# Optimization experiments

Hardware: AMD Instinct MI355X
Metric: run time of the kernel (lower is better)

Reference implementation:

```python
import jax, jax.numpy as jnp
import numpy as np
from jax import lax

D = 256; NH = 8; LYR = 2; G = 64; K = G * G; T = 4; EC = 32
B = 4; N = 512; CITY = 256; DFF = 4 * D

def _conv(x, w):
    return lax.conv_general_dilated(x, w, (1, 1), 'SAME', dimension_numbers=('NCHW', 'OIHW', 'NCHW'))

def _ln(x, w, b):
    m = x.mean(-1, keepdims=True)
    v = ((x - m) ** 2).mean(-1, keepdims=True)
    return (x - m) / jnp.sqrt(v + 1e-5) * w + b

def _mlp(x, w1, b1, w2, b2):
    return jax.nn.gelu(x @ w1 + b1) @ w2 + b2

def setup_inputs():
    key = jax.random.key(0)
    ks = iter(jax.random.split(key, 64))
    def nrm(shape, s=0.02):
        return jax.random.normal(next(ks), shape, jnp.float32) * s
    return {
        'meas_xy': jax.random.uniform(next(ks), (B, N, 2), jnp.float32),
        'meas_v': jax.random.normal(next(ks), (B, N), jnp.float32),
        'bs_xy': jax.random.uniform(next(ks), (B, 1, 2), jnp.float32),
        'task_id': jax.random.randint(next(ks), (B,), 0, T),
        'city': jax.random.uniform(next(ks), (B, CITY, CITY), jnp.float32),
        'mp_w1': nrm((3, D)), 'mp_b1': jnp.zeros((D,)), 'mp_w2': nrm((D, D)), 'mp_b2': jnp.zeros((D,)),
        'bp_w1': nrm((2, D)), 'bp_b1': jnp.zeros((D,)), 'bp_w2': nrm((D, D)), 'bp_b2': jnp.zeros((D,)),
        'env_w1': nrm((EC, 1, 3, 3)), 'env_b1': jnp.zeros((EC,)),
        'env_w2': nrm((EC, EC, 3, 3)), 'env_b2': jnp.zeros((EC,)),
        'env_w3': nrm((D, EC, 1, 1)), 'env_b3': jnp.zeros((D,)),
        'task_emb': nrm((T, D)), 'tp_w': nrm((D, D)), 'tp_b': jnp.zeros((D,)),
        'grid_pos': nrm((K, D)),
        'blk_dens_w': nrm((LYR, D)), 'blk_dens_b': jnp.zeros((LYR, D)),
        'blk_ln1_w': jnp.ones((LYR, D)), 'blk_ln1_b': jnp.zeros((LYR, D)),
        'blk_wq': nrm((LYR, D, D)), 'blk_bq': jnp.zeros((LYR, D)),
        'blk_wk': nrm((LYR, D, D)), 'blk_bk': jnp.zeros((LYR, D)),
        'blk_wv': nrm((LYR, D, D)), 'blk_bv': jnp.zeros((LYR, D)),
        'blk_wo': nrm((LYR, D, D)), 'blk_bo': jnp.zeros((LYR, D)),
        'blk_ln2_w': jnp.ones((LYR, D)), 'blk_ln2_b': jnp.zeros((LYR, D)),
        'blk_ff_w1': nrm((LYR, D, DFF)), 'blk_ff_b1': jnp.zeros((LYR, DFF)),
        'blk_ff_w2': nrm((LYR, DFF, D)), 'blk_ff_b2': jnp.zeros((LYR, D)),
        'tfp_w': nrm((T, D, D)), 'tfp_b': jnp.zeros((T, D)),
        'head_w': nrm((D, 1)), 'head_b': jnp.zeros((1,)),
    }

def reference(meas_xy, meas_v, bs_xy, task_id, city, mp_w1, mp_b1, mp_w2, mp_b2, bp_w1, bp_b1, bp_w2, bp_b2, env_w1, env_b1, env_w2, env_b2, env_w3, env_b3, task_emb, tp_w, tp_b, grid_pos, blk_dens_w, blk_dens_b, blk_ln1_w, blk_ln1_b, blk_wq, blk_bq, blk_wk, blk_bk, blk_wv, blk_bv, blk_wo, blk_bo, blk_ln2_w, blk_ln2_b, blk_ff_w1, blk_ff_b1, blk_ff_w2, blk_ff_b2, tfp_w, tfp_b, head_w, head_b):
    b = meas_xy.shape[0]
    dh = D // NH
    # normalized grid cell centers, [K,2] in (x,y) order
    c = (jnp.arange(G, dtype=jnp.float32) + 0.5) / G
    gy, gx = jnp.meshgrid(c, c, indexing='ij')
    grid_xy = jnp.stack([gx, gy], -1).reshape(K, 2)
    meas_tok = _mlp(jnp.concatenate([meas_xy, meas_v[..., None]], -1), mp_w1, mp_b1, mp_w2, mp_b2)
    bs_tok = _mlp(bs_xy, bp_w1, bp_b1, bp_w2, bp_b2)
    src = jnp.concatenate([meas_tok, bs_tok], 1)       # [B,Ns,D]
    src_xy = jnp.concatenate([meas_xy, bs_xy], 1)      # [B,Ns,2]
    # distance bias: [B,K,Ns]
    attn_bias = -jnp.linalg.norm(grid_xy[None, :, None, :] - src_xy[:, None, :, :], axis=-1)
    # gaussian measurement density: [B,K]
    diff = grid_xy[None, :, None, :] - meas_xy[:, None, :, :]
    dist2 = (diff * diff).sum(-1)
    sigma = 0.08
    density = jnp.exp(-dist2 / (2.0 * sigma * sigma)).mean(-1)
    # env branch: nearest-resize city to GxG, small CNN
    idx = jnp.floor(jnp.arange(G) * (city.shape[1] / G)).astype(jnp.int32)
    city_grid = city[:, idx][:, :, idx][:, None]       # [B,1,G,G]
    h = jax.nn.gelu(_conv(city_grid, env_w1) + env_b1[None, :, None, None])
    h = jax.nn.gelu(_conv(h, env_w2) + env_b2[None, :, None, None])
    env_map = _conv(h, env_w3) + env_b3[None, :, None, None]
    env_grid = env_map.transpose(0, 2, 3, 1).reshape(b, K, D)
    task_vec = (task_emb[task_id] @ tp_w + tp_b)[:, None, :]
    grid = grid_pos[None] + task_vec + env_grid
    inv_sqrt = jnp.float32(1.0 / np.sqrt(dh))
    for l in range(LYR):
        # density modulation injected into the grid latent
        g = grid + density[..., None] * blk_dens_w[l] + blk_dens_b[l]
        hn = _ln(g, blk_ln1_w[l], blk_ln1_b[l])
        q = (hn @ blk_wq[l] + blk_bq[l]).reshape(b, K, NH, dh)
        kk = (src @ blk_wk[l] + blk_bk[l]).reshape(b, -1, NH, dh)
        vv = (src @ blk_wv[l] + blk_bv[l]).reshape(b, -1, NH, dh)
        scores = jnp.einsum('bkhd,bnhd->bhkn', q, kk) * inv_sqrt + attn_bias[:, None]
        a = jax.nn.softmax(scores, -1)
        o = jnp.einsum('bhkn,bnhd->bkhd', a, vv).reshape(b, K, D) @ blk_wo[l] + blk_bo[l]
        g = g + o
        g = g + _mlp(_ln(g, blk_ln2_w[l], blk_ln2_b[l]), blk_ff_w1[l], blk_ff_b1[l], blk_ff_w2[l], blk_ff_b2[l])
        grid = g
    # per-sample task projection from the weight bank
    tf = jax.nn.gelu(jnp.einsum('bkd,bdh->bkh', grid, tfp_w[task_id]) + tfp_b[task_id][:, None, :])
    logits = (tf @ head_w + head_b)[..., 0].reshape(b, G, G)
    return logits
```

## Files before the change

### kernel.cpp

```cpp
#include <hip/hip_runtime.h>
#include <hip/hip_bf16.h>
#include <math.h>

#define D 256
#define NH 8
#define DH 32
#define LYR 2
#define G 64
#define KK 4096
#define T 4
#define EC 32
#define B 4
#define N 512
#define CITY 256
#define DFF 1024
#define NS 513
#define NSP 544
#define MSRC 2052
#define MSRCP 2176
#define ISQ 0.17677669529663687f
#define LOG2E 1.4426950408889634f

typedef short bf16x8 __attribute__((ext_vector_type(8)));
typedef float f32x4 __attribute__((ext_vector_type(4)));

__device__ __forceinline__ float gelu_f(float x) {
    const float c2 = 2.f * 0.7978845608028654f * LOG2E;
    float u = x + 0.044715f * x * x * x;
    float e = __builtin_amdgcn_exp2f(-c2 * u);
    return x * __builtin_amdgcn_rcpf(1.f + e);
}

__device__ __forceinline__ unsigned short f2bf(float f) {
    unsigned int u = __float_as_uint(f);
    unsigned int r = (u + 0x7FFFu + ((u >> 16) & 1u)) >> 16;
    return (unsigned short)r;
}

__device__ __forceinline__ float bf2f(unsigned short u) {
    return __uint_as_float((unsigned)u << 16);
}

__device__ __forceinline__ unsigned cvtpk(float a, float b) {
    unsigned r;
    asm("v_cvt_pk_bf16_f32 %0, %1, %2" : "=v"(r) : "v"(a), "v"(b));
    return r;
}

__device__ __forceinline__ void gl2lds16(const unsigned short* g, unsigned short* l) {
    __builtin_amdgcn_global_load_lds(
        (const __attribute__((address_space(1))) unsigned int*)g,
        (__attribute__((address_space(3))) unsigned int*)l, 16, 0, 0);
}

__global__ __launch_bounds__(256) void pre1_k(
    const float* __restrict__ wq, const float* __restrict__ wk,
    const float* __restrict__ wv, const float* __restrict__ wo,
    const float* __restrict__ ff1, const float* __restrict__ ff2,
    const float* __restrict__ tfp,
    const float* __restrict__ bk, const float* __restrict__ bv,
    unsigned short* __restrict__ wqT, unsigned short* __restrict__ kvT,
    unsigned short* __restrict__ woT, unsigned short* __restrict__ ff1T,
    unsigned short* __restrict__ ff2T, unsigned short* __restrict__ tfpT,
    float* __restrict__ kvbias,
    const float* __restrict__ meas_xy, const float* __restrict__ meas_v,
    const float* __restrict__ bs_xy,
    const float* __restrict__ mp_w1, const float* __restrict__ mp_b1,
    const float* __restrict__ mp_w2, const float* __restrict__ mp_b2,
    const float* __restrict__ bp_w1, const float* __restrict__ bp_b1,
    const float* __restrict__ bp_w2, const float* __restrict__ bp_b2,
    unsigned short* __restrict__ srcbf, float* __restrict__ src_xy,
    float* __restrict__ dens,
    const float* __restrict__ city, const float* __restrict__ env_w1,
    const float* __restrict__ env_b1, float* __restrict__ h1,
    const float* __restrict__ task_emb, const int* __restrict__ task_id,
    const float* __restrict__ tp_w, const float* __restrict__ tp_b,
    float* __restrict__ tvec,
    unsigned short* __restrict__ khd, unsigned short* __restrict__ vch)
{
    __shared__ float sh[1088];
    int bx = blockIdx.x;
    int tid = threadIdx.x;
    if (bx < 1792) {
        const float* src; unsigned short* dst;
        int Kd, Nn, nmat, rowOff = 0, t; size_t matStride;
        if (bx < 512) {
            int job = bx >> 7; t = bx & 127;
            Kd = 256; Nn = 256; nmat = 2;
            if (job == 0)      { src = wq; dst = wqT; matStride = 65536; }
            else if (job == 1) { src = wk; dst = kvT; matStride = 131072; }
            else if (job == 2) { src = wv; dst = kvT; matStride = 131072; rowOff = 256; }
            else               { src = wo; dst = woT; matStride = 65536; }
            if ((t & 63) == 0 && job == 1) kvbias[(t >> 6) * 512 + tid] = bk[(t >> 6) * 256 + tid];
            if ((t & 63) == 0 && job == 2) kvbias[(t >> 6) * 512 + 256 + tid] = bv[(t >> 6) * 256 + tid];
        } else if (bx < 1024) { t = bx - 512;  src = ff1; dst = ff1T; Kd = 256;  Nn = 1024; nmat = 2; matStride = 262144; }
        else if (bx < 1536)   { t = bx - 1024; src = ff2; dst = ff2T; Kd = 1024; Nn = 256;  nmat = 2; matStride = 262144; }
        else                  { t = bx - 1536; src = tfp; dst = tfpT; Kd = 256;  Nn = 256;  nmat = 4; matStride = 65536; }
        int tn = Nn / 32, perMat = tn * (Kd / 32);
        int mat = t / perMat;
        int rem = t - mat * perMat;
        int nb = (rem % tn) * 32, kb = (rem / tn) * 32;
        const float* s = src + (size_t)mat * Kd * Nn;
        unsigned short* d = dst + (size_t)mat * matStride;
        float (*tb)[33] = (float (*)[33])sh;
        int tx = tid & 31, ty = tid >> 5;
        #pragma unroll
        for (int i = 0; i < 4; i++)
            tb[ty + i * 8][tx] = s[(size_t)(kb + ty + i * 8) * Nn + nb + tx];
        __syncthreads();
        #pragma unroll
        for (int i = 0; i < 4; i++)
            d[(size_t)(rowOff + nb + ty + i * 8) * Kd + kb + tx] = f2bf(tb[tx][ty + i * 8]);
    } else if (bx < 3968) {
        int id = bx - 1792;
        int dd = tid;
        if (id >= B * N + B) {
            srcbf[(size_t)id * D + dd] = 0;
            return;
        }
        float* hid = sh;
        int row;
        const float *w1, *b1, *w2, *b2;
        float x0, x1, x2 = 0.f;
        int nin;
        if (id < B * N) {
            int b = id >> 9, n = id & 511;
            x0 = meas_xy[(b * N + n) * 2 + 0];
            x1 = meas_xy[(b * N + n) * 2 + 1];
            x2 = meas_v[b * N + n];
            w1 = mp_w1; b1 = mp_b1; w2 = mp_w2; b2 = mp_b2; nin = 3;
            row = b * NS + n;
        } else {
            int b = id - B * N;
            x0 = bs_xy[b * 2 + 0];
            x1 = bs_xy[b * 2 + 1];
            w1 = bp_w1; b1 = bp_b1; w2 = bp_w2; b2 = bp_b2; nin = 2;
            row = b * NS + N;
        }
        float h = x0 * w1[dd] + x1 * w1[D + dd] + b1[dd];
        if (nin == 3) h += x2 * w1[2 * D + dd];
        hid[dd] = gelu_f(h);
        __syncthreads();
        float o = b2[dd];
        for (int j = 0; j < D; j++) o += hid[j] * w2[j * D + dd];
        srcbf[(size_t)row * D + dd] = f2bf(o);
        if (dd == 0) { src_xy[row * 2 + 0] = x0; src_xy[row * 2 + 1] = x1; }
    } else if (bx < 4032) {
        int blk = bx - 3968;
        int b = blk >> 4, kc = blk & 15;
        int k = kc * 256 + tid;
        float* mx = sh; float* my = sh + 512;
        for (int i = tid; i < N; i += 256) {
            mx[i] = meas_xy[(b * N + i) * 2 + 0];
            my[i] = meas_xy[(b * N + i) * 2 + 1];
        }
        __syncthreads();
        float gx = ((k & 63) + 0.5f) / 64.f;
        float gy = ((k >> 6) + 0.5f) / 64.f;
        float s = 0.f;
        for (int n = 0; n < N; n++) {
            float dx = gx - mx[n], dy = gy - my[n];
            s += __expf(-(dx * dx + dy * dy) * 78.125f);
        }
        dens[b * KK + k] = s * (1.f / (float)N);
    } else if (bx < 6080) {
        int i = (bx - 4032) * 256 + tid;
        int x = i & 63, y = (i >> 6) & 63, c = (i >> 12) & 31, b = i >> 17;
        float s = env_b1[c];
        for (int ky = 0; ky < 3; ky++) {
            int yy = y + ky - 1;
            if (yy < 0 || yy >= G) continue;
            for (int kx = 0; kx < 3; kx++) {
                int xx = x + kx - 1;
                if (xx < 0 || xx >= G) continue;
                s += city[(b * CITY + yy * 4) * CITY + xx * 4] * env_w1[c * 9 + ky * 3 + kx];
            }
        }
        h1[i] = gelu_f(s);
    } else if (bx < 6084) {
        int b = bx - 6080;
        float* e = sh;
        e[tid] = task_emb[task_id[b] * D + tid];
        __syncthreads();
        float s = tp_b[tid];
        for (int j = 0; j < D; j++) s += e[j] * tp_w[j * D + tid];
        tvec[b * D + tid] = s;
    } else {
        int bh = bx - 6084;
        unsigned short* kp = khd + ((size_t)bh * 544 + 513) * 32;
        for (int i = tid; i < 992; i += 256) kp[i] = 0;
        unsigned short* vp = vch + ((size_t)bh * 17 + 16) * 1024;
        for (int i = tid; i < 1024; i += 256) vp[i] = 0;
    }
}

__global__ __launch_bounds__(256) void conv2_k(
    const float* __restrict__ h1, const float* __restrict__ w,
    const float* __restrict__ bias, float* __restrict__ h2) {
    int blk = blockIdx.x;
    int yt = blk & 15, cg = (blk >> 4) & 7, b = blk >> 7;
    int x = threadIdx.x & 63, y = yt * 4 + (threadIdx.x >> 6);
    int c0 = cg * 4;
    float flag[9];
    int off[9];
    #pragma unroll
    for (int ky = 0; ky < 3; ky++) {
        int yy = y + ky - 1;
        bool vy = (yy >= 0 && yy < G);
        int yc = min(max(yy, 0), G - 1);
        #pragma unroll
        for (int kx = 0; kx < 3; kx++) {
            int xx = x + kx - 1;
            bool vx = (xx >= 0 && xx < G);
            int xc = min(max(xx, 0), G - 1);
            flag[ky * 3 + kx] = (vy && vx) ? 1.f : 0.f;
            off[ky * 3 + kx] = yc * G + xc;
        }
    }
    const float* hp = h1 + ((size_t)(b * EC) << 12);
    float acc[4] = {bias[c0], bias[c0 + 1], bias[c0 + 2], bias[c0 + 3]};
    float v[9], nv[9];
    #pragma unroll
    for (int t = 0; t < 9; t++) v[t] = hp[off[t]] * flag[t];
    for (int ci = 0; ci < EC; ci++) {
        if (ci < EC - 1) {
            const float* hn = hp + ((size_t)(ci + 1) << 12);
            #pragma unroll
            for (int t = 0; t < 9; t++) nv[t] = hn[off[t]] * flag[t];
        }
        #pragma unroll
        for (int cc = 0; cc < 4; cc++) {
            const float* wp = w + ((size_t)(c0 + cc) * EC + ci) * 9;
            #pragma unroll
            for (int t = 0; t < 9; t++) acc[cc] += v[t] * wp[t];
        }
        #pragma unroll
        for (int t = 0; t < 9; t++) v[t] = nv[t];
    }
    size_t obase = (((size_t)(b * EC + c0)) << 12) + y * G + x;
    #pragma unroll
    for (int cc = 0; cc < 4; cc++)
        h2[obase + ((size_t)cc << 12)] = gelu_f(acc[cc]);
}

__global__ __launch_bounds__(256) void pre2_k(
    const float* __restrict__ h2, const float* __restrict__ w3,
    const float* __restrict__ b3, const float* __restrict__ grid_pos,
    const float* __restrict__ tvec, float* __restrict__ grid,
    float* __restrict__ out, const float* __restrict__ head_b)
{
    __shared__ float sh[1088];
    int bx = blockIdx.x;
    int tid = threadIdx.x;
    if (bx < 2048) {
        int b = bx >> 9, k0 = (bx & 511) * 8;
        float (*h2s)[8] = (float (*)[8])sh;
        h2s[tid >> 3][tid & 7] = h2[(((size_t)b * EC + (tid >> 3)) << 12) + k0 + (tid & 7)];
        float w3r[32];
        #pragma unroll
        for (int c4 = 0; c4 < 8; c4++) {
            float4 w4 = *(const float4*)(w3 + tid * 32 + c4 * 4);
            w3r[c4 * 4 + 0] = w4.x; w3r[c4 * 4 + 1] = w4.y;
            w3r[c4 * 4 + 2] = w4.z; w3r[c4 * 4 + 3] = w4.w;
        }
        float base = b3[tid] + tvec[b * D + tid];
        __syncthreads();
        #pragma unroll
        for (int j = 0; j < 8; j++) {
            float s = base + grid_pos[(size_t)(k0 + j) * D + tid];
            #pragma unroll
            for (int ci = 0; ci < 32; ci++) s += h2s[ci][j] * w3r[ci];
            grid[((size_t)b * KK + k0 + j) * D + tid] = s;
        }
    } else {
        out[(bx - 2048) * 256 + tid] = head_b[0];
    }
}

template <int DENS>
__global__ __launch_bounds__(256) void dens_ln_k(
    float* __restrict__ grid, const float* __restrict__ dens,
    const float* __restrict__ dw, const float* __restrict__ db,
    const float* __restrict__ lw, const float* __restrict__ lb,
    unsigned short* __restrict__ y) {
    int row = blockIdx.x * 4 + (threadIdx.x >> 6);
    int lane = threadIdx.x & 63;
    float* gp = grid + (size_t)row * D + lane * 4;
    float4 v = *(float4*)gp;
    if (DENS) {
        float de = dens[row];
        float4 w4 = *(const float4*)(dw + lane * 4);
        float4 b4 = *(const float4*)(db + lane * 4);
        v.x += de * w4.x + b4.x; v.y += de * w4.y + b4.y;
        v.z += de * w4.z + b4.z; v.w += de * w4.w + b4.w;
        *(float4*)gp = v;
    }
    float s = v.x + v.y + v.z + v.w;
    #pragma unroll
    for (int o = 32; o > 0; o >>= 1) s += __shfl_xor(s, o);
    float mean = s * (1.f / D);
    float cx = v.x - mean, cy = v.y - mean, cz = v.z - mean, cw = v.w - mean;
    float q = cx * cx + cy * cy + cz * cz + cw * cw;
    #pragma unroll
    for (int o = 32; o > 0; o >>= 1) q += __shfl_xor(q, o);
    float inv = rsqrtf(q * (1.f / D) + 1e-5f);
    float4 lwv = *(const float4*)(lw + lane * 4);
    float4 lbv = *(const float4*)(lb + lane * 4);
    ushort4 o4;
    o4.x = f2bf(cx * inv * lwv.x + lbv.x);
    o4.y = f2bf(cy * inv * lwv.y + lbv.y);
    o4.z = f2bf(cz * inv * lwv.z + lbv.z);
    o4.w = f2bf(cw * inv * lwv.w + lbv.w);
    *(ushort4*)(y + (size_t)row * D + lane * 4) = o4;
}

template <int GELU, int ACCUM, int OBF, int TFPH, int STBF, int KVT = 0>
__device__ __forceinline__ void gemm_core(
    const unsigned short* __restrict__ A, const unsigned short* __restrict__ Wt,
    const float* __restrict__ bias, void* __restrict__ Cv,
    int M, int K, int Nn, int bn, int bm,
    const float* __restrict__ hw, unsigned short* __restrict__ Xb, float scale,
    unsigned short* As, unsigned short* Bs) {
    int tid = threadIdx.x;
    int wave = tid >> 6, lane = tid & 63;
    int q4 = lane >> 4, lr = lane & 15;
    int wn = wave * 16;
    int srow = tid >> 2;
    int sk8 = ((tid & 3) ^ ((tid >> 3) & 3)) * 8;
    const unsigned short* Ap  = A  + (size_t)(bm + srow) * K + sk8;
    const unsigned short* Bp0 = Wt + (size_t)(bn + srow) * K + sk8;
    unsigned short* AsD = As + tid * 8;
    unsigned short* BsD = Bs + tid * 8;
    int q4x = (q4 ^ ((lr >> 1) & 3)) * 8;
    f32x4 acc[4] = {};

    gl2lds16(Ap,       AsD);
    gl2lds16(Ap + 32,  AsD + 2048);
    gl2lds16(Bp0,      BsD);
    gl2lds16(Bp0 + 32, BsD + 2048);

    int nk = K >> 6;
    for (int ki = 0; ki < nk; ki++) {
        __syncthreads();
        if (ki + 1 < nk) {
            int k0 = (ki + 1) << 6;
            int nb = ((ki + 1) & 1) * 4096;
            gl2lds16(Ap + k0,       AsD + nb);
            gl2lds16(Ap + k0 + 32,  AsD + nb + 2048);
            gl2lds16(Bp0 + k0,      BsD + nb);
            gl2lds16(Bp0 + k0 + 32, BsD + nb + 2048);
        }
        int cb = (ki & 1) * 4096;
        #pragma unroll
        for (int ks = 0; ks < 2; ks++) {
            bf16x8 af[4], bf;
            #pragma unroll
            for (int i = 0; i < 4; i++)
                af[i] = *(const bf16x8*)&As[cb + ks * 2048 + (i * 16 + lr) * 32 + q4x];
            bf = *(const bf16x8*)&Bs[cb + ks * 2048 + (wn + lr) * 32 + q4x];
            #pragma unroll
            for (int i = 0; i < 4; i++)
                acc[i] = __builtin_amdgcn_mfma_f32_16x16x32_bf16(af[i], bf, acc[i], 0, 0, 0);
        }
    }

    if (KVT) {
        int gc = bn + wn + lr;
        float bv = bias[gc];
        bool isV = gc >= 256;
        #pragma unroll
        for (int i = 0; i < 4; i++) {
            #pragma unroll
            for (int r = 0; r < 4; r++) {
                int gr = bm + i * 16 + q4 * 4 + r;
                if (gr < MSRC) {
                    float v = acc[i][r] + bv;
                    int bb = gr / NS;
                    int tok = gr - bb * NS;
                    if (!isV) {
                        int h = gc >> 5, dh = gc & 31;
                        int t32 = tok & 31;
                        int kkp = ((t32 & 1) << 4) | ((t32 >> 3) << 2) | ((t32 >> 1) & 3);
                        int tokP = (tok & ~31) | kkp;
                        ((unsigned short*)Cv)[(((size_t)(bb * 8 + h) * 544) + tokP) * 32 + dh] = f2bf(v);
                    } else {
                        int gcv = gc - 256;
                        int h = gcv >> 5, dh = gcv & 31;
                        int c = tok >> 5, t32 = tok & 31;
                        Xb[((((size_t)(bb * 8 + h) * 17 + c) * 32 + dh)) * 32 + t32] = f2bf(v);
                    }
                }
            }
        }
        return;
    }

    if (TFPH) {
        int gc = bn + wn + lr;
        float bv = bias[gc];
        float hv = hw[gc];
        #pragma unroll
        for (int i = 0; i < 4; i++) {
            #pragma unroll
            for (int r = 0; r < 4; r++) {
                float s = gelu_f(acc[i][r] + bv) * hv;
                s += __shfl_xor(s, 1); s += __shfl_xor(s, 2);
                s += __shfl_xor(s, 4); s += __shfl_xor(s, 8);
                if (lr == 0)
                    atomicAdd((float*)Cv + (bm + i * 16 + q4 * 4 + r), s);
            }
        }
        return;
    }

    int gc = bn + wn + lr;
    float bv = bias[gc];
    #pragma unroll
    for (int i = 0; i < 4; i++) {
        #pragma unroll
        for (int r = 0; r < 4; r++) {
            int gr = bm + i * 16 + q4 * 4 + r;
            if (gr < M) {
                float v = (acc[i][r] + bv) * scale;
                if (GELU) v = gelu_f(v);
                size_t idx = (size_t)gr * Nn + gc;
                if (OBF) {
                    ((unsigned short*)Cv)[idx] = f2bf(v);
                } else if (ACCUM) {
                    float nv = ((float*)Cv)[idx] + v;
                    ((float*)Cv)[idx] = nv;
                    if (STBF) Xb[idx] = f2bf(nv);
                } else {
                    ((float*)Cv)[idx] = v;
                }
            }
        }
    }
}

template <int GELU, int ACCUM, int OBF, int TFPH, int STBF>
__global__ __launch_bounds__(256) void gemm_k(
    const unsigned short* __restrict__ A, const unsigned short* __restrict__ Wt0,
    const float* __restrict__ bias0, void* __restrict__ Cv,
    int M, int K, int Nn, const int* __restrict__ task_id,
    const float* __restrict__ hw, unsigned short* __restrict__ Xb) {
    __shared__ unsigned short As[8192];
    __shared__ unsigned short Bs[8192];
    const unsigned short* Wt = Wt0;
    const float* bias = bias0;
    int bm = blockIdx.y * 64;
    if (TFPH) { int t = task_id[bm >> 12]; Wt += (size_t)t * D * D; bias += t * D; }
    gemm_core<GELU, ACCUM, OBF, TFPH, STBF>(A, Wt, bias, Cv, M, K, Nn,
                                            blockIdx.x * 64, bm, hw, Xb, 1.f, As, Bs);
}

template <int GELU, int ACCUM, int OBF, int STBF>
__global__ __launch_bounds__(256) void gemm128_k(
    const unsigned short* __restrict__ A, const unsigned short* __restrict__ Wt,
    const float* __restrict__ bias, void* __restrict__ Cv,
    int M, int K, int Nn, unsigned short* __restrict__ Xb) {
    __shared__ unsigned short As[16384];
    __shared__ unsigned short Bs[8192];
    int tid = threadIdx.x;
    int wave = tid >> 6, lane = tid & 63;
    int q4 = lane >> 4, lr = lane & 15;
    int wn = wave * 16;
    int bn = blockIdx.x * 64, bm = blockIdx.y * 128;
    int srow = tid >> 2;
    int sk8 = ((tid & 3) ^ ((tid >> 3) & 3)) * 8;
    const unsigned short* Ap  = A + (size_t)(bm + srow) * K + sk8;
    const unsigned short* Ap2 = Ap + (size_t)64 * K;
    const unsigned short* Bp  = Wt + (size_t)(bn + srow) * K + sk8;
    unsigned short* AsD = As + tid * 8;
    unsigned short* BsD = Bs + tid * 8;
    int q4x = (q4 ^ ((lr >> 1) & 3)) * 8;
    f32x4 acc[8] = {};

    gl2lds16(Ap,        AsD);
    gl2lds16(Ap2,       AsD + 2048);
    gl2lds16(Ap + 32,   AsD + 4096);
    gl2lds16(Ap2 + 32,  AsD + 6144);
    gl2lds16(Bp,        BsD);
    gl2lds16(Bp + 32,   BsD + 2048);

    int nk = K >> 6;
    for (int ki = 0; ki < nk; ki++) {
        __syncthreads();
        if (ki + 1 < nk) {
            int k0 = (ki + 1) << 6;
            int nbA = ((ki + 1) & 1) * 8192;
            int nbB = ((ki + 1) & 1) * 4096;
            gl2lds16(Ap + k0,        AsD + nbA);
            gl2lds16(Ap2 + k0,       AsD + nbA + 2048);
            gl2lds16(Ap + k0 + 32,   AsD + nbA + 4096);
            gl2lds16(Ap2 + k0 + 32,  AsD + nbA + 6144);
            gl2lds16(Bp + k0,        BsD + nbB);
            gl2lds16(Bp + k0 + 32,   BsD + nbB + 2048);
        }
        int cbA = (ki & 1) * 8192, cbB = (ki & 1) * 4096;
        #pragma unroll
        for (int ks = 0; ks < 2; ks++) {
            bf16x8 bf = *(const bf16x8*)&Bs[cbB + ks * 2048 + (wn + lr) * 32 + q4x];
            #pragma unroll
            for (int i = 0; i < 8; i++) {
                bf16x8 af = *(const bf16x8*)&As[cbA + ks * 4096 + (i * 16 + lr) * 32 + q4x];
                acc[i] = __builtin_amdgcn_mfma_f32_16x16x32_bf16(af, bf, acc[i], 0, 0, 0);
            }
        }
    }

    int gc = bn + wn + lr;
    float bv = bias[gc];
    #pragma unroll
    for (int i = 0; i < 8; i++) {
        #pragma unroll
        for (int r = 0; r < 4; r++) {
            int gr = bm + i * 16 + q4 * 4 + r;
            float v = acc[i][r] + bv;
            if (GELU) v = gelu_f(v);
            size_t idx = (size_t)gr * Nn + gc;
            if (OBF) {
                ((unsigned short*)Cv)[idx] = f2bf(v);
            } else if (ACCUM) {
                float nv = ((float*)Cv)[idx] + v;
                ((float*)Cv)[idx] = nv;
                if (STBF) Xb[idx] = f2bf(nv);
            } else {
                ((float*)Cv)[idx] = v;
            }
        }
    }
}

__global__ __launch_bounds__(256) void qkv_k(
    const unsigned short* __restrict__ xbf, const unsigned short* __restrict__ wqT,
    const float* __restrict__ bq, unsigned short* __restrict__ qbf,
    const unsigned short* __restrict__ srcbf, const unsigned short* __restrict__ kvT,
    const float* __restrict__ kvb, unsigned short* __restrict__ khd,
    unsigned short* __restrict__ vch) {
    __shared__ unsigned short As[8192];
    __shared__ unsigned short Bs[8192];
    if (blockIdx.x < 4) {
        gemm_core<0, 0, 1, 0, 0, 0>(xbf, wqT, bq, qbf, B * KK, D, D,
                                    blockIdx.x * 64, blockIdx.y * 64, nullptr, nullptr,
                                    ISQ * LOG2E, As, Bs);
    } else {
        if (blockIdx.y >= MSRCP / 64) return;
        gemm_core<0, 0, 1, 0, 0, 1>(srcbf, kvT, kvb, khd, MSRC, D, 512,
                                    (blockIdx.x - 4) * 64, blockIdx.y * 64, nullptr, vch, 1.f, As, Bs);
    }
}

__global__ __launch_bounds__(256) void attn_mfma(
    const unsigned short* __restrict__ qb,
    const unsigned short* __restrict__ khd,
    const unsigned short* __restrict__ vch,
    const float* __restrict__ sxy,
    unsigned short* __restrict__ out)
{
    __shared__ float2 sxys[NSP];
    int bid = blockIdx.x;
    int qt = bid & 63, h = (bid >> 6) & 7, b = bid >> 9;
    int tid = threadIdx.x, wave = tid >> 6, lane = tid & 63;
    int q4 = lane >> 4, lr = lane & 15;

    int kbase = qt * 64 + wave * 16;
    size_t qrow = (size_t)(b * KK + kbase + lr);
    bf16x8 qf = *(const bf16x8*)(qb + qrow * D + h * DH + q4 * 8);
    const unsigned short* kp0 = khd + ((size_t)(b * 8 + h) * 544) * 32 + lr * 32 + q4 * 8;
    const unsigned short* vb0 = vch + ((size_t)(b * 8 + h) * 17) * 1024 + lr * 32 + q4 * 8;

    float ll0 = 0.f, ll1 = 0.f;
    f32x4 o0 = {0.f, 0.f, 0.f, 0.f}, o1 = {0.f, 0.f, 0.f, 0.f};

    bf16x8 k0X, k1X, v0X, v1X, k0Y, k1Y, v0Y, v1Y;
    f32x4 d0X, d1X, d0Y, d1Y;

#define LDK(S, c) { size_t co = (size_t)(c) * 1024; \
    k0##S = *(const bf16x8*)(kp0 + co); k1##S = *(const bf16x8*)(kp0 + co + 512); }
#define LDV(S, c) { size_t co = (size_t)(c) * 1024; \
    v0##S = *(const bf16x8*)(vb0 + co); v1##S = *(const bf16x8*)(vb0 + co + 512); }

    LDK(X, 0); LDV(X, 0);
    LDK(Y, 1); LDV(Y, 1);

    float gy = (qt + 0.5f) * (1.f / 64.f);
    const float2* sb = (const float2*)(sxy + 2 * (size_t)b * NS);
    for (int i = tid; i < NSP; i += 256) {
        float2 v = (i < NS) ? sb[i] : make_float2(1.e4f, 1.e4f);
        float ey = (gy - v.y) * LOG2E;
        sxys[i] = make_float2(v.x * LOG2E, ey * ey);
    }
    __syncthreads();

    int qi = wave * 16 + lr;
    float gxp = (qi + 0.5f) * (1.f / 64.f) * LOG2E;
    const float2* spf = &sxys[q4 * 8];

#define DIST(xx, yy2) ({ float dx_ = gxp - (xx); \
    __builtin_amdgcn_sqrtf(__builtin_fmaf(dx_, dx_, (yy2))); })
#define LDB(S, c) { const float4* p4_ = (const float4*)(spf + (size_t)(c) * 32); \
    float4 a0_ = p4_[0], a1_ = p4_[1], a2_ = p4_[2], a3_ = p4_[3]; \
    d0##S[0] = DIST(a0_.x, a0_.y); d1##S[0] = DIST(a0_.z, a0_.w); \
    d0##S[1] = DIST(a1_.x, a1_.y); d1##S[1] = DIST(a1_.z, a1_.w); \
    d0##S[2] = DIST(a2_.x, a2_.y); d1##S[2] = DIST(a2_.z, a2_.w); \
    d0##S[3] = DIST(a3_.x, a3_.y); d1##S[3] = DIST(a3_.z, a3_.w); }

    LDB(X, 0); LDB(Y, 1);

#define BODY(S, cp) { \
    f32x4 s0 = {0.f, 0.f, 0.f, 0.f}, s1 = {0.f, 0.f, 0.f, 0.f}; \
    s0 = __builtin_amdgcn_mfma_f32_16x16x32_bf16(k0##S, qf, s0, 0, 0, 0); \
    s1 = __builtin_amdgcn_mfma_f32_16x16x32_bf16(k1##S, qf, s1, 0, 0, 0); \
    LDK(S, cp); \
    float p0[4], p1[4]; \
    p0[0] = __builtin_amdgcn_exp2f(s0[0] - d0##S[0]); \
    p0[1] = __builtin_amdgcn_exp2f(s0[1] - d0##S[1]); \
    p0[2] = __builtin_amdgcn_exp2f(s0[2] - d0##S[2]); \
    p0[3] = __builtin_amdgcn_exp2f(s0[3] - d0##S[3]); \
    p1[0] = __builtin_amdgcn_exp2f(s1[0] - d1##S[0]); \
    p1[1] = __builtin_amdgcn_exp2f(s1[1] - d1##S[1]); \
    p1[2] = __builtin_amdgcn_exp2f(s1[2] - d1##S[2]); \
    p1[3] = __builtin_amdgcn_exp2f(s1[3] - d1##S[3]); \
    LDB(S, cp); \
    ll0 += (p0[0] + p0[1]) + (p0[2] + p0[3]); \
    ll1 += (p1[0] + p1[1]) + (p1[2] + p1[3]); \
    union { unsigned u[4]; bf16x8 v; } pu; \
    pu.u[0] = cvtpk(p0[0], p1[0]); \
    pu.u[1] = cvtpk(p0[1], p1[1]); \
    pu.u[2] = cvtpk(p0[2], p1[2]); \
    pu.u[3] = cvtpk(p0[3], p1[3]); \
    o0 = __builtin_amdgcn_mfma_f32_16x16x32_bf16(v0##S, pu.v, o0, 0, 0, 0); \
    o1 = __builtin_amdgcn_mfma_f32_16x16x32_bf16(v1##S, pu.v, o1, 0, 0, 0); \
    LDV(S, cp); \
}

    for (int c = 0; c < 16; c += 2) {
        int cpX = c + 2;
        int cpY = (c + 3 > 16) ? 16 : c + 3;
        BODY(X, cpX);
        BODY(Y, cpY);
    }
    BODY(X, 16);

#undef BODY
#undef LDB
#undef DIST
#undef LDK
#undef LDV

    float ll = ll0 + ll1;
    ll += __shfl_xor(ll, 16);
    ll += __shfl_xor(ll, 32);
    float inv = 1.f / ll;
    unsigned w0 = cvtpk(o0[0] * inv, o0[1] * inv);
    unsigned w1 = cvtpk(o0[2] * inv, o0[3] * inv);
    unsigned w2 = cvtpk(o1[0] * inv, o1[1] * inv);
    unsigned w3 = cvtpk(o1[2] * inv, o1[3] * inv);
    uint2 st0; st0.x = w0; st0.y = w1;
    uint2 st1; st1.x = w2; st1.y = w3;
    *(uint2*)(out + qrow * D + h * DH + q4 * 4) = st0;
    *(uint2*)(out + qrow * D + h * DH + 16 + q4 * 4) = st1;
}

extern "C" void kernel_launch(void* const* d_in, const int* in_sizes, int n_in,
                              void* d_out, int out_size, void* d_ws, size_t ws_size,
                              hipStream_t stream) {
    const float* meas_xy = (const float*)d_in[0];
    const float* meas_v  = (const float*)d_in[1];
    const float* bs_xy   = (const float*)d_in[2];
    const int*   task_id = (const int*)d_in[3];
    const float* city    = (const float*)d_in[4];
    const float* mp_w1 = (const float*)d_in[5];  const float* mp_b1 = (const float*)d_in[6];
    const float* mp_w2 = (const float*)d_in[7];  const float* mp_b2 = (const float*)d_in[8];
    const float* bp_w1 = (const float*)d_in[9];  const float* bp_b1 = (const float*)d_in[10];
    const float* bp_w2 = (const float*)d_in[11]; const float* bp_b2 = (const float*)d_in[12];
    const float* env_w1 = (const float*)d_in[13]; const float* env_b1 = (const float*)d_in[14];
    const float* env_w2 = (const float*)d_in[15]; const float* env_b2 = (const float*)d_in[16];
    const float* env_w3 = (const float*)d_in[17]; const float* env_b3 = (const float*)d_in[18];
    const float* task_emb = (const float*)d_in[19];
    const float* tp_w = (const float*)d_in[20]; const float* tp_b = (const float*)d_in[21];
    const float* grid_pos = (const float*)d_in[22];
    const float* dens_w = (const float*)d_in[23]; const float* dens_b = (const float*)d_in[24];
    const float* ln1_w = (const float*)d_in[25]; const float* ln1_b = (const float*)d_in[26];
    const float* wq = (const float*)d_in[27]; const float* bq = (const float*)d_in[28];
    const float* wk = (const float*)d_in[29]; const float* bk = (const float*)d_in[30];
    const float* wv = (const float*)d_in[31]; const float* bv = (const float*)d_in[32];
    const float* wo = (const float*)d_in[33]; const float* bo = (const float*)d_in[34];
    const float* ln2_w = (const float*)d_in[35]; const float* ln2_b = (const float*)d_in[36];
    const float* ff_w1 = (const float*)d_in[37]; const float* ff_b1 = (const float*)d_in[38];
    const float* ff_w2 = (const float*)d_in[39]; const float* ff_b2 = (const float*)d_in[40];
    const float* tfp_w = (const float*)d_in[41]; const float* tfp_b = (const float*)d_in[42];
    const float* head_w = (const float*)d_in[43]; const float* head_b = (const float*)d_in[44];
    float* out = (float*)d_out;

    float* ws = (float*)d_ws;
    size_t off = 0;
    float* src_xy = ws + off; off += (size_t)B * NS * 2 + 128;
    float* dens   = ws + off; off += (size_t)B * KK;
    float* tvec   = ws + off; off += (size_t)B * D;
    float* h1     = ws + off; off += (size_t)B * EC * KK;
    float* grid   = ws + off; off += (size_t)B * KK * D;
    unsigned short* srcbf = (unsigned short*)(ws + off); off += (size_t)MSRCP * D / 2;
    unsigned short* khd   = (unsigned short*)(ws + off); off += (size_t)B * 8 * 544 * 32 / 2;
    unsigned short* vch   = (unsigned short*)(ws + off); off += (size_t)B * 8 * 17 * 1024 / 2;
    float* qreg   = ws + off; off += (size_t)B * KK * D / 2;
    unsigned short* qbf = (unsigned short*)qreg;
    float* h2     = qreg;
    unsigned short* xbf    = (unsigned short*)(ws + off); off += (size_t)B * KK * D / 2;
    unsigned short* attnbf = (unsigned short*)(ws + off); off += (size_t)B * KK * D / 2;
    unsigned short* hidbf  = (unsigned short*)(ws + off); off += (size_t)B * KK * DFF / 2;
    unsigned short* wqT  = (unsigned short*)(ws + off); off += (size_t)LYR * D * D / 2;
    unsigned short* kvT  = (unsigned short*)(ws + off); off += (size_t)LYR * 512 * D / 2;
    unsigned short* woT  = (unsigned short*)(ws + off); off += (size_t)LYR * D * D / 2;
    unsigned short* ff1T = (unsigned short*)(ws + off); off += (size_t)LYR * D * DFF / 2;
    unsigned short* ff2T = (unsigned short*)(ws + off); off += (size_t)LYR * DFF * D / 2;
    unsigned short* tfpT = (unsigned short*)(ws + off); off += (size_t)T * D * D / 2;
    float* kvbias = ws + off; off += (size_t)LYR * 512;
    (void)ws_size; (void)n_in; (void)in_sizes; (void)out_size;

    const int M = B * KK;

    pre1_k<<<6116, 256, 0, stream>>>(
        wq, wk, wv, wo, ff_w1, ff_w2, tfp_w, bk, bv,
        wqT, kvT, woT, ff1T, ff2T, tfpT, kvbias,
        meas_xy, meas_v, bs_xy, mp_w1, mp_b1, mp_w2, mp_b2,
        bp_w1, bp_b1, bp_w2, bp_b2, srcbf, src_xy,
        dens, city, env_w1, env_b1, h1,
        task_emb, task_id, tp_w, tp_b, tvec, khd, vch);
    conv2_k<<<512, 256, 0, stream>>>(h1, env_w2, env_b2, h2);
    pre2_k<<<2112, 256, 0, stream>>>(h2, env_w3, env_b3, grid_pos, tvec, grid,
                                     out, head_b);

    for (int l = 0; l < LYR; l++) {
        dens_ln_k<1><<<M / 4, 256, 0, stream>>>(grid, dens, dens_w + l * D, dens_b + l * D,
                                                ln1_w + l * D, ln1_b + l * D, xbf);
        qkv_k<<<dim3(12, 256), 256, 0, stream>>>(
            xbf, wqT + (size_t)l * D * D, bq + l * D, qbf,
            srcbf, kvT + (size_t)l * 512 * D, kvbias + l * 512, khd, vch);
        attn_mfma<<<B * NH * 64, 256, 0, stream>>>(qbf, khd, vch, src_xy, attnbf);
        gemm128_k<0, 1, 0, 0><<<dim3(4, 128), 256, 0, stream>>>(
            attnbf, woT + (size_t)l * D * D, bo + l * D, grid, M, D, D, nullptr);
        dens_ln_k<0><<<M / 4, 256, 0, stream>>>(grid, nullptr, nullptr, nullptr,
                                                ln2_w + l * D, ln2_b + l * D, xbf);
        gemm128_k<1, 0, 1, 0><<<dim3(16, 128), 256, 0, stream>>>(
            xbf, ff1T + (size_t)l * D * DFF, ff_b1 + l * DFF, hidbf, M, D, DFF, nullptr);
        if (l == 0) {
            gemm128_k<0, 1, 0, 0><<<dim3(4, 128), 256, 0, stream>>>(
                hidbf, ff2T + (size_t)l * DFF * D, ff_b2 + l * D, grid, M, DFF, D, nullptr);
        } else {
            gemm128_k<0, 1, 0, 1><<<dim3(4, 128), 256, 0, stream>>>(
                hidbf, ff2T + (size_t)l * DFF * D, ff_b2 + l * D, grid, M, DFF, D, xbf);
        }
    }
    gemm_k<1, 0, 0, 1, 0><<<dim3(4, 256), 256, 0, stream>>>(
        xbf, tfpT, tfp_b, out, M, D, D, task_id, head_w, nullptr);
}
```

Measured before the change: 531.5 us.

## Process two query rows per attention block to reuse K/V loads

Each attention block now handles two adjacent grid rows (two query tiles) instead of one, so every K/V chunk loaded is used for twice as many MFMA score and PV products. The distance bias is computed for both rows from a shared dx term, and the LDS source table now stores raw scaled coordinates instead of a per-row squared dy. The grid is halved to 1024 blocks, which cuts K/V global traffic but doubles register pressure per thread and lowers the number of blocks available to fill the GPU.

```diff
diff --git a/kernel.cpp b/kernel.cpp
--- a/kernel.cpp
+++ b/kernel.cpp
@@ -560,21 +560,26 @@
 {
     __shared__ float2 sxys[NSP];
     int bid = blockIdx.x;
-    int qt = bid & 63, h = (bid >> 6) & 7, b = bid >> 9;
+    int qp = bid & 31, h = (bid >> 5) & 7, b = bid >> 8;
+    int qt0 = qp * 2;
     int tid = threadIdx.x, wave = tid >> 6, lane = tid & 63;
     int q4 = lane >> 4, lr = lane & 15;
 
-    int kbase = qt * 64 + wave * 16;
-    size_t qrow = (size_t)(b * KK + kbase + lr);
-    bf16x8 qf = *(const bf16x8*)(qb + qrow * D + h * DH + q4 * 8);
+    int cell0 = qt0 * 64 + wave * 16 + lr;
+    size_t qrow0 = (size_t)(b * KK + cell0);
+    size_t qrow1 = qrow0 + 64;
+    bf16x8 qfA = *(const bf16x8*)(qb + qrow0 * D + h * DH + q4 * 8);
+    bf16x8 qfB = *(const bf16x8*)(qb + qrow1 * D + h * DH + q4 * 8);
     const unsigned short* kp0 = khd + ((size_t)(b * 8 + h) * 544) * 32 + lr * 32 + q4 * 8;
     const unsigned short* vb0 = vch + ((size_t)(b * 8 + h) * 17) * 1024 + lr * 32 + q4 * 8;
 
-    float ll0 = 0.f, ll1 = 0.f;
-    f32x4 o0 = {0.f, 0.f, 0.f, 0.f}, o1 = {0.f, 0.f, 0.f, 0.f};
+    float lla0 = 0.f, lla1 = 0.f, llb0 = 0.f, llb1 = 0.f;
+    f32x4 o0a = {0.f, 0.f, 0.f, 0.f}, o1a = {0.f, 0.f, 0.f, 0.f};
+    f32x4 o0b = {0.f, 0.f, 0.f, 0.f}, o1b = {0.f, 0.f, 0.f, 0.f};
 
     bf16x8 k0X, k1X, v0X, v1X, k0Y, k1Y, v0Y, v1Y;
     f32x4 d0X, d1X, d0Y, d1Y;
+    f32x4 e0X, e1X, e0Y, e1Y;
 
 #define LDK(S, c) { size_t co = (size_t)(c) * 1024; \
     k0##S = *(const bf16x8*)(kp0 + co); k1##S = *(const bf16x8*)(kp0 + co + 512); }
@@ -584,54 +589,74 @@
     LDK(X, 0); LDV(X, 0);
     LDK(Y, 1); LDV(Y, 1);
 
-    float gy = (qt + 0.5f) * (1.f / 64.f);
     const float2* sb = (const float2*)(sxy + 2 * (size_t)b * NS);
     for (int i = tid; i < NSP; i += 256) {
         float2 v = (i < NS) ? sb[i] : make_float2(1.e4f, 1.e4f);
-        float ey = (gy - v.y) * LOG2E;
-        sxys[i] = make_float2(v.x * LOG2E, ey * ey);
+        sxys[i] = make_float2(v.x * LOG2E, v.y * LOG2E);
     }
     __syncthreads();
 
     int qi = wave * 16 + lr;
-    float gxp = (qi + 0.5f) * (1.f / 64.f) * LOG2E;
+    float gxp  = (qi + 0.5f) * (1.f / 64.f) * LOG2E;
+    float gy0p = (qt0 + 0.5f) * (1.f / 64.f) * LOG2E;
+    float gy1p = (qt0 + 1.5f) * (1.f / 64.f) * LOG2E;
     const float2* spf = &sxys[q4 * 8];
 
-#define DIST(xx, yy2) ({ float dx_ = gxp - (xx); \
-    __builtin_amdgcn_sqrtf(__builtin_fmaf(dx_, dx_, (yy2))); })
+#define DIST2(xx, yy, dq0, dq1) { float dx_ = gxp - (xx); float dx2_ = dx_ * dx_; \
+    float dy0_ = gy0p - (yy); dq0 = __builtin_amdgcn_sqrtf(__builtin_fmaf(dy0_, dy0_, dx2_)); \
+    float dy1_ = gy1p - (yy); dq1 = __builtin_amdgcn_sqrtf(__builtin_fmaf(dy1_, dy1_, dx2_)); }
 #define LDB(S, c) { const float4* p4_ = (const float4*)(spf + (size_t)(c) * 32); \
     float4 a0_ = p4_[0], a1_ = p4_[1], a2_ = p4_[2], a3_ = p4_[3]; \
-    d0##S[0] = DIST(a0_.x, a0_.y); d1##S[0] = DIST(a0_.z, a0_.w); \
-    d0##S[1] = DIST(a1_.x, a1_.y); d1##S[1] = DIST(a1_.z, a1_.w); \
-    d0##S[2] = DIST(a2_.x, a2_.y); d1##S[2] = DIST(a2_.z, a2_.w); \
-    d0##S[3] = DIST(a3_.x, a3_.y); d1##S[3] = DIST(a3_.z, a3_.w); }
+    DIST2(a0_.x, a0_.y, d0##S[0], e0##S[0]); DIST2(a0_.z, a0_.w, d1##S[0], e1##S[0]); \
+    DIST2(a1_.x, a1_.y, d0##S[1], e0##S[1]); DIST2(a1_.z, a1_.w, d1##S[1], e1##S[1]); \
+    DIST2(a2_.x, a2_.y, d0##S[2], e0##S[2]); DIST2(a2_.z, a2_.w, d1##S[2], e1##S[2]); \
+    DIST2(a3_.x, a3_.y, d0##S[3], e0##S[3]); DIST2(a3_.z, a3_.w, d1##S[3], e1##S[3]); }
 
     LDB(X, 0); LDB(Y, 1);
 
 #define BODY(S, cp) { \
-    f32x4 s0 = {0.f, 0.f, 0.f, 0.f}, s1 = {0.f, 0.f, 0.f, 0.f}; \
-    s0 = __builtin_amdgcn_mfma_f32_16x16x32_bf16(k0##S, qf, s0, 0, 0, 0); \
-    s1 = __builtin_amdgcn_mfma_f32_16x16x32_bf16(k1##S, qf, s1, 0, 0, 0); \
+    f32x4 s0a = {0.f, 0.f, 0.f, 0.f}, s1a = {0.f, 0.f, 0.f, 0.f}; \
+    f32x4 s0b = {0.f, 0.f, 0.f, 0.f}, s1b = {0.f, 0.f, 0.f, 0.f}; \
+    s0a = __builtin_amdgcn_mfma_f32_16x16x32_bf16(k0##S, qfA, s0a, 0, 0, 0); \
+    s1a = __builtin_amdgcn_mfma_f32_16x16x32_bf16(k1##S, qfA, s1a, 0, 0, 0); \
+    s0b = __builtin_amdgcn_mfma_f32_16x16x32_bf16(k0##S, qfB, s0b, 0, 0, 0); \
+    s1b = __builtin_amdgcn_mfma_f32_16x16x32_bf16(k1##S, qfB, s1b, 0, 0, 0); \
     LDK(S, cp); \
-    float p0[4], p1[4]; \
-    p0[0] = __builtin_amdgcn_exp2f(s0[0] - d0##S[0]); \
-    p0[1] = __builtin_amdgcn_exp2f(s0[1] - d0##S[1]); \
-    p0[2] = __builtin_amdgcn_exp2f(s0[2] - d0##S[2]); \
-    p0[3] = __builtin_amdgcn_exp2f(s0[3] - d0##S[3]); \
-    p1[0] = __builtin_amdgcn_exp2f(s1[0] - d1##S[0]); \
-    p1[1] = __builtin_amdgcn_exp2f(s1[1] - d1##S[1]); \
-    p1[2] = __builtin_amdgcn_exp2f(s1[2] - d1##S[2]); \
-    p1[3] = __builtin_amdgcn_exp2f(s1[3] - d1##S[3]); \
+    float p0a[4], p1a[4], p0b[4], p1b[4]; \
+    p0a[0] = __builtin_amdgcn_exp2f(s0a[0] - d0##S[0]); \
+    p0a[1] = __builtin_amdgcn_exp2f(s0a[1] - d0##S[1]); \
+    p0a[2] = __builtin_amdgcn_exp2f(s0a[2] - d0##S[2]); \
+    p0a[3] = __builtin_amdgcn_exp2f(s0a[3] - d0##S[3]); \
+    p1a[0] = __builtin_amdgcn_exp2f(s1a[0] - d1##S[0]); \
+    p1a[1] = __builtin_amdgcn_exp2f(s1a[1] - d1##S[1]); \
+    p1a[2] = __builtin_amdgcn_exp2f(s1a[2] - d1##S[2]); \
+    p1a[3] = __builtin_amdgcn_exp2f(s1a[3] - d1##S[3]); \
+    p0b[0] = __builtin_amdgcn_exp2f(s0b[0] - e0##S[0]); \
+    p0b[1] = __builtin_amdgcn_exp2f(s0b[1] - e0##S[1]); \
+    p0b[2] = __builtin_amdgcn_exp2f(s0b[2] - e0##S[2]); \
+    p0b[3] = __builtin_amdgcn_exp2f(s0b[3] - e0##S[3]); \
+    p1b[0] = __builtin_amdgcn_exp2f(s1b[0] - e1##S[0]); \
+    p1b[1] = __builtin_amdgcn_exp2f(s1b[1] - e1##S[1]); \
+    p1b[2] = __builtin_amdgcn_exp2f(s1b[2] - e1##S[2]); \
+    p1b[3] = __builtin_amdgcn_exp2f(s1b[3] - e1##S[3]); \
     LDB(S, cp); \
-    ll0 += (p0[0] + p0[1]) + (p0[2] + p0[3]); \
-    ll1 += (p1[0] + p1[1]) + (p1[2] + p1[3]); \
-    union { unsigned u[4]; bf16x8 v; } pu; \
-    pu.u[0] = cvtpk(p0[0], p1[0]); \
-    pu.u[1] = cvtpk(p0[1], p1[1]); \
-    pu.u[2] = cvtpk(p0[2], p1[2]); \
-    pu.u[3] = cvtpk(p0[3], p1[3]); \
-    o0 = __builtin_amdgcn_mfma_f32_16x16x32_bf16(v0##S, pu.v, o0, 0, 0, 0); \
-    o1 = __builtin_amdgcn_mfma_f32_16x16x32_bf16(v1##S, pu.v, o1, 0, 0, 0); \
+    lla0 += (p0a[0] + p0a[1]) + (p0a[2] + p0a[3]); \
+    lla1 += (p1a[0] + p1a[1]) + (p1a[2] + p1a[3]); \
+    llb0 += (p0b[0] + p0b[1]) + (p0b[2] + p0b[3]); \
+    llb1 += (p1b[0] + p1b[1]) + (p1b[2] + p1b[3]); \
+    union { unsigned u[4]; bf16x8 v; } pua, pub; \
+    pua.u[0] = cvtpk(p0a[0], p1a[0]); \
+    pua.u[1] = cvtpk(p0a[1], p1a[1]); \
+    pua.u[2] = cvtpk(p0a[2], p1a[2]); \
+    pua.u[3] = cvtpk(p0a[3], p1a[3]); \
+    pub.u[0] = cvtpk(p0b[0], p1b[0]); \
+    pub.u[1] = cvtpk(p0b[1], p1b[1]); \
+    pub.u[2] = cvtpk(p0b[2], p1b[2]); \
+    pub.u[3] = cvtpk(p0b[3], p1b[3]); \
+    o0a = __builtin_amdgcn_mfma_f32_16x16x32_bf16(v0##S, pua.v, o0a, 0, 0, 0); \
+    o1a = __builtin_amdgcn_mfma_f32_16x16x32_bf16(v1##S, pua.v, o1a, 0, 0, 0); \
+    o0b = __builtin_amdgcn_mfma_f32_16x16x32_bf16(v0##S, pub.v, o0b, 0, 0, 0); \
+    o1b = __builtin_amdgcn_mfma_f32_16x16x32_bf16(v1##S, pub.v, o1b, 0, 0, 0); \
     LDV(S, cp); \
 }
 
@@ -645,22 +670,31 @@
 
 #undef BODY
 #undef LDB
-#undef DIST
+#undef DIST2
 #undef LDK
 #undef LDV
 
-    float ll = ll0 + ll1;
-    ll += __shfl_xor(ll, 16);
-    ll += __shfl_xor(ll, 32);
-    float inv = 1.f / ll;
-    unsigned w0 = cvtpk(o0[0] * inv, o0[1] * inv);
-    unsigned w1 = cvtpk(o0[2] * inv, o0[3] * inv);
-    unsigned w2 = cvtpk(o1[0] * inv, o1[1] * inv);
-    unsigned w3 = cvtpk(o1[2] * inv, o1[3] * inv);
-    uint2 st0; st0.x = w0; st0.y = w1;
-    uint2 st1; st1.x = w2; st1.y = w3;
-    *(uint2*)(out + qrow * D + h * DH + q4 * 4) = st0;
-    *(uint2*)(out + qrow * D + h * DH + 16 + q4 * 4) = st1;
+    float lla = lla0 + lla1;
+    lla += __shfl_xor(lla, 16);
+    lla += __shfl_xor(lla, 32);
+    float inva = 1.f / lla;
+    float llb = llb0 + llb1;
+    llb += __shfl_xor(llb, 16);
+    llb += __shfl_xor(llb, 32);
+    float invb = 1.f / llb;
+    uint2 sa0, sa1, sb0, sb1;
+    sa0.x = cvtpk(o0a[0] * inva, o0a[1] * inva);
+    sa0.y = cvtpk(o0a[2] * inva, o0a[3] * inva);
+    sa1.x = cvtpk(o1a[0] * inva, o1a[1] * inva);
+    sa1.y = cvtpk(o1a[2] * inva, o1a[3] * inva);
+    sb0.x = cvtpk(o0b[0] * invb, o0b[1] * invb);
+    sb0.y = cvtpk(o0b[2] * invb, o0b[3] * invb);
+    sb1.x = cvtpk(o1b[0] * invb, o1b[1] * invb);
+    sb1.y = cvtpk(o1b[2] * invb, o1b[3] * invb);
+    *(uint2*)(out + qrow0 * D + h * DH + q4 * 4) = sa0;
+    *(uint2*)(out + qrow0 * D + h * DH + 16 + q4 * 4) = sa1;
+    *(uint2*)(out + qrow1 * D + h * DH + q4 * 4) = sb0;
+    *(uint2*)(out + qrow1 * D + h * DH + 16 + q4 * 4) = sb1;
 }
 
 extern "C" void kernel_launch(void* const* d_in, const int* in_sizes, int n_in,
@@ -738,7 +772,7 @@
         qkv_k<<<dim3(12, 256), 256, 0, stream>>>(
             xbf, wqT + (size_t)l * D * D, bq + l * D, qbf,
             srcbf, kvT + (size_t)l * 512 * D, kvbias + l * 512, khd, vch);
-        attn_mfma<<<B * NH * 64, 256, 0, stream>>>(qbf, khd, vch, src_xy, attnbf);
+        attn_mfma<<<B * NH * 32, 256, 0, stream>>>(qbf, khd, vch, src_xy, attnbf);
         gemm128_k<0, 1, 0, 0><<<dim3(4, 128), 256, 0, stream>>>(
             attnbf, woT + (size_t)l * D * D, bo + l * D, grid, M, D, D, nullptr);
         dens_ln_k<0><<<M / 4, 256, 0, stream>>>(grid, nullptr, nullptr, nullptr,
```

Measured after the change: 517.8 us. 1.03x faster.
